# Kernel tuning notes

Hardware: AMD Instinct MI355X
Metric: run time of the kernel (lower is better)

Reference implementation:

```python
import jax, jax.numpy as jnp
import numpy as np

N, P, C = 100000, 48, 8
D, H = 64, 4
DH = D // H
FLAG = 7
EPS = 1e-5


def _layer_norm(x, g, b):
    mu = x.mean(-1, keepdims=True)
    var = ((x - mu) ** 2).mean(-1, keepdims=True)
    return (x - mu) * jax.lax.rsqrt(var + EPS) * g + b


def setup_inputs() -> dict:
    key = jax.random.key(0)
    ks = jax.random.split(key, 24)
    w = lambda k, shp: (jax.random.normal(k, shp, dtype=jnp.float32) * 0.05)
    inp = {
        "voxel_features": jax.random.normal(ks[0], (N, D), dtype=jnp.float32),
        "voxels": jax.random.normal(ks[1], (N, P, C), dtype=jnp.float32),
        "pp_w1": w(ks[2], (D, C)), "pp_b1": w(ks[3], (D,)),
        "pp_w2": w(ks[4], (D, D)), "pp_b2": w(ks[5], (D,)),
        "in_proj_w": w(ks[6], (3 * D, D)), "in_proj_b": w(ks[7], (3 * D,)),
        "out_w": w(ks[8], (D, D)), "out_b": w(ks[9], (D,)),
        "ln1_g": jnp.ones((D,), jnp.float32), "ln1_b": jnp.zeros((D,), jnp.float32),
        "ffn_w1": w(ks[10], (2 * D, D)), "ffn_b1": w(ks[11], (2 * D,)),
        "ffn_w2": w(ks[12], (D, 2 * D)), "ffn_b2": w(ks[13], (D,)),
        "ln2_g": jnp.ones((D,), jnp.float32), "ln2_b": jnp.zeros((D,), jnp.float32),
        "op_w1": w(ks[14], (D, D)), "op_b1": w(ks[15], (D,)),
        "op_w2": w(ks[16], (D, D)), "op_b2": w(ks[17], (D,)),
        "num_points": jax.random.randint(ks[18], (N,), 0, P, dtype=jnp.int32),
    }
    return inp


def reference(voxel_features, voxels, pp_w1, pp_b1, pp_w2, pp_b2,
              in_proj_w, in_proj_b, out_w, out_b, ln1_g, ln1_b,
              ffn_w1, ffn_b1, ffn_w2, ffn_b2, ln2_g, ln2_b,
              op_w1, op_b1, op_w2, op_b2, num_points):
    n, p, _ = voxels.shape
    point_mask = jnp.arange(p)[None, :] < num_points[:, None]          # [N,P]
    current_mask = (voxels[:, :, FLAG] > 0.5) & point_mask             # [N,P]
    history_mask = point_mask & ~current_mask                          # [N,P]
    history_present = history_mask.any(axis=1, keepdims=True)          # [N,1]

    point_features = voxels[:, :, :C]

    def masked_mean(vals, mask):
        m = mask.astype(vals.dtype)[..., None]
        counts = jnp.clip(mask.sum(1, keepdims=True), 1, None).astype(vals.dtype)
        return (vals * m).sum(1) / counts                              # [N,C]

    cur_sum = masked_mean(point_features, current_mask)
    his_sum = masked_mean(point_features, history_mask)

    def point_proj(x):
        return jax.nn.relu(x @ pp_w1.T + pp_b1) @ pp_w2.T + pp_b2

    tokens = jnp.stack([voxel_features, point_proj(cur_sum), point_proj(his_sum)], axis=1)  # [N,3,D]

    key_pad = jnp.stack([jnp.zeros((n,), bool),
                         ~current_mask.any(1),
                         ~history_present[:, 0]], axis=1)              # [N,3]

    # multi-head self-attention over 3 tokens
    qkv = tokens @ in_proj_w.T + in_proj_b                             # [N,3,3D]
    q, k, v = jnp.split(qkv, 3, axis=-1)
    q = q.reshape(n, 3, H, DH).transpose(0, 2, 1, 3)                   # [N,H,3,DH]
    k = k.reshape(n, 3, H, DH).transpose(0, 2, 1, 3)
    v = v.reshape(n, 3, H, DH).transpose(0, 2, 1, 3)
    scores = jnp.einsum('nhqd,nhkd->nhqk', q, k) / np.sqrt(DH)
    scores = jnp.where(key_pad[:, None, None, :], -jnp.inf, scores)
    attn = jax.nn.softmax(scores, axis=-1)
    ctx = jnp.einsum('nhqk,nhkd->nhqd', attn, v)                       # [N,H,3,DH]
    ctx = ctx.transpose(0, 2, 1, 3).reshape(n, 3, D)
    attn_out = ctx @ out_w.T + out_b

    tokens = _layer_norm(tokens + attn_out, ln1_g, ln1_b)
    ffn = jax.nn.relu(tokens @ ffn_w1.T + ffn_b1) @ ffn_w2.T + ffn_b2
    tokens = _layer_norm(tokens + ffn, ln2_g, ln2_b)

    refined = jax.nn.relu(tokens[:, 0] @ op_w1.T + op_b1) @ op_w2.T + op_b2
    refined = refined * history_present.astype(refined.dtype)
    return voxel_features + refined
```

## Files before the change

kernel.cpp:

```cpp
#include <hip/hip_runtime.h>


using bf16x8 = __attribute__((ext_vector_type(8))) __bf16;
using f32x4  = __attribute__((ext_vector_type(4))) float;

#define DEV static __device__ __forceinline__

DEV float bf2f(unsigned short u){
  union { unsigned int i; float f; } v; v.i = ((unsigned int)u) << 16; return v.f;
}
DEV unsigned short f2bf(float f){
  union { float f; unsigned int i; } v; v.f = f;
  unsigned int x = v.i;
  x += 0x7FFFu + ((x >> 16) & 1u);
  return (unsigned short)(x >> 16);
}

DEV unsigned short* lp(unsigned short* base, int row, int col){
  int byte = (col << 1) ^ ((row & 7) << 4);
  return (unsigned short*)((char*)base + (row << 7) + byte);
}

DEV bf16x8 ldA(const unsigned short* base, int mt, int kt, int lane){
  int row = mt*16 + (lane & 15);
  int col = kt*32 + ((lane >> 4) << 3);
  return *(const bf16x8*)lp((unsigned short*)base, row, col);
}
DEV bf16x8 ldB(const unsigned short* w, int frag, int lane){
  return *(const bf16x8*)(w + (size_t)frag*512 + (size_t)lane*8);
}
DEV void stC(unsigned short* base, int mt, int nt, f32x4 c, int lane){
  int col  = nt*16 + (lane & 15);
  int row0 = mt*16 + ((lane >> 4) << 2);
  #pragma unroll
  for (int r = 0; r < 4; ++r) *lp(base, row0 + r, col) = f2bf(c[r]);
}
DEV f32x4 MF(bf16x8 a, bf16x8 b, f32x4 c){
  return __builtin_amdgcn_mfma_f32_16x16x32_bf16(a, b, c, 0, 0, 0);
}

DEV void ld16(const unsigned short* base, int row, int col0, float* o){
  uint4 a = *(const uint4*)lp((unsigned short*)base, row, col0);
  uint4 b = *(const uint4*)lp((unsigned short*)base, row, col0 + 8);
  unsigned int w[8] = {a.x, a.y, a.z, a.w, b.x, b.y, b.z, b.w};
  #pragma unroll
  for (int i = 0; i < 8; ++i){
    union { unsigned int u; float f; } lo, hi;
    lo.u = w[i] << 16; hi.u = w[i] & 0xFFFF0000u;
    o[2*i] = lo.f; o[2*i+1] = hi.f;
  }
}
DEV void st16(unsigned short* base, int row, int col0, const float* f){
  unsigned int w[8];
  #pragma unroll
  for (int i = 0; i < 8; ++i)
    w[i] = (unsigned int)f2bf(f[2*i]) | ((unsigned int)f2bf(f[2*i+1]) << 16);
  *(uint4*)lp(base, row, col0)     = make_uint4(w[0], w[1], w[2], w[3]);
  *(uint4*)lp(base, row, col0 + 8) = make_uint4(w[4], w[5], w[6], w[7]);
}

DEV bf16x8 pack8(const float* f){
  union { bf16x8 v; unsigned short u[8]; } r;
  #pragma unroll
  for (int i = 0; i < 8; ++i) r.u[i] = f2bf(f[i]);
  return r.v;
}

DEV void layer_norm16(f32x4 x[4], const float* g, const float* b, int lane){
  float s[4], s2[4];
  #pragma unroll
  for (int r = 0; r < 4; ++r){
    s[r]  = x[0][r] + x[1][r] + x[2][r] + x[3][r];
    s2[r] = x[0][r]*x[0][r] + x[1][r]*x[1][r] + x[2][r]*x[2][r] + x[3][r]*x[3][r];
  }
  #pragma unroll
  for (int o = 1; o <= 8; o <<= 1){
    #pragma unroll
    for (int r = 0; r < 4; ++r){
      s[r]  += __shfl_xor(s[r],  o);
      s2[r] += __shfl_xor(s2[r], o);
    }
  }
  float mu[4], rs[4];
  #pragma unroll
  for (int r = 0; r < 4; ++r){
    mu[r] = s[r] * (1.f/64.f);
    float var = s2[r] * (1.f/64.f) - mu[r]*mu[r];
    rs[r] = rsqrtf(var + 1e-5f);
  }
  const int cl = lane & 15;
  #pragma unroll
  for (int nt = 0; nt < 4; ++nt){
    float gg = g[nt*16 + cl], bb = b[nt*16 + cl];
    #pragma unroll
    for (int r = 0; r < 4; ++r)
      x[nt][r] = (x[nt][r] - mu[r]) * rs[r] * gg + bb;
  }
}

__global__ void tva_pack_weights(const float* __restrict__ pp_w1, const float* __restrict__ pp_w2,
                                 const float* __restrict__ in_proj_w, const float* __restrict__ out_w,
                                 const float* __restrict__ ffn_w1, const float* __restrict__ ffn_w2,
                                 const float* __restrict__ op_w1, const float* __restrict__ op_w2,
                                 unsigned short* __restrict__ ws)
{
  int b = blockIdx.x, lane = threadIdx.x;
  const float* W; int base, ktiles, K;
  if      (b < 4)  { W = pp_w1;     base = 0;  ktiles = 1; K = 8;   }
  else if (b < 12) { W = pp_w2;     base = 4;  ktiles = 2; K = 64;  }
  else if (b < 36) { W = in_proj_w; base = 12; ktiles = 2; K = 64;  }
  else if (b < 44) { W = out_w;     base = 36; ktiles = 2; K = 64;  }
  else if (b < 60) { W = ffn_w1;    base = 44; ktiles = 2; K = 64;  }
  else if (b < 76) { W = ffn_w2;    base = 60; ktiles = 4; K = 128; }
  else if (b < 84) { W = op_w1;     base = 76; ktiles = 2; K = 64;  }
  else             { W = op_w2;     base = 84; ktiles = 2; K = 64;  }
  int local = b - base;
  int nt = local / ktiles, kt = local % ktiles;
  int n  = nt*16 + (lane & 15);
  int k0 = kt*32 + ((lane >> 4) << 3);
  unsigned short* dst = ws + (size_t)b*512 + (size_t)lane*8;
  #pragma unroll
  for (int i = 0; i < 8; ++i){
    int k = k0 + i;
    float v = (k < K) ? W[(size_t)n*K + k] : 0.0f;
    dst[i] = f2bf(v);
  }
}

__global__ __launch_bounds__(256)
void tva_main(const float* __restrict__ vf, const float* __restrict__ vox,
              const int* __restrict__ num_points,
              const float* __restrict__ pp_b1, const float* __restrict__ pp_b2,
              const float* __restrict__ ipb,  const float* __restrict__ outb,
              const float* __restrict__ ln1g, const float* __restrict__ ln1b,
              const float* __restrict__ f1b,  const float* __restrict__ f2bv,
              const float* __restrict__ ln2g, const float* __restrict__ ln2b,
              const float* __restrict__ o1b,  const float* __restrict__ o2b,
              const unsigned short* __restrict__ wfrag,
              float* __restrict__ out, int nvox)
{
  __shared__ unsigned short smem[4 * 64 * 64];
  const int tid  = threadIdx.x;
  const int wv   = tid >> 6;
  const int lane = tid & 63;
  unsigned short* X = smem + wv * (64*64);
  unsigned short* Q = X + 48*64;

  const int v0 = (blockIdx.x * 4 + wv) * 16;
  if (v0 >= nvox) return;
  const int cl = lane & 15;
  const int r0 = (lane >> 4) << 2;

  const int vi = lane >> 2, pq = lane & 3;
  const int np = num_points[v0 + vi];
  float cs[8] = {0,0,0,0,0,0,0,0}, hs[8] = {0,0,0,0,0,0,0,0};
  float cc = 0.f, hc = 0.f;
  const float4* vp = (const float4*)(vox + (size_t)(v0 + vi) * 384);
  #pragma unroll
  for (int k = 0; k < 12; ++k){
    int p = pq + (k << 2);
    float4 a = vp[p*2], b = vp[p*2 + 1];
    float pm = (p < np) ? 1.f : 0.f;
    float cm = (b.w > 0.5f) ? pm : 0.f;
    float hm = pm - cm;
    cc += cm; hc += hm;
    cs[0] += a.x*cm; cs[1] += a.y*cm; cs[2] += a.z*cm; cs[3] += a.w*cm;
    cs[4] += b.x*cm; cs[5] += b.y*cm; cs[6] += b.z*cm; cs[7] += b.w*cm;
    hs[0] += a.x*hm; hs[1] += a.y*hm; hs[2] += a.z*hm; hs[3] += a.w*hm;
    hs[4] += b.x*hm; hs[5] += b.y*hm; hs[6] += b.z*hm; hs[7] += b.w*hm;
  }
  #pragma unroll
  for (int o = 1; o <= 2; o <<= 1){
    cc += __shfl_xor(cc, o); hc += __shfl_xor(hc, o);
    #pragma unroll
    for (int j = 0; j < 8; ++j){
      cs[j] += __shfl_xor(cs[j], o);
      hs[j] += __shfl_xor(hs[j], o);
    }
  }
  const float icc = 1.f / fmaxf(cc, 1.f);
  const float ihc = 1.f / fmaxf(hc, 1.f);
  const unsigned int myfw = (cc > 0.f ? 1u : 0u) | (hc > 0.f ? 2u : 0u);

  bf16x8 ac, ah;
  {
    const int src = cl * 4;
    float cf[8], hf[8];
    #pragma unroll
    for (int i = 0; i < 8; ++i){
      cf[i] = __shfl(cs[i]*icc, src);
      hf[i] = __shfl(hs[i]*ihc, src);
    }
    union { bf16x8 v; unsigned short u[8]; } rc, rh;
    #pragma unroll
    for (int i = 0; i < 8; ++i){
      rc.u[i] = (lane < 16) ? f2bf(cf[i]) : (unsigned short)0;
      rh.u[i] = (lane < 16) ? f2bf(hf[i]) : (unsigned short)0;
    }
    ac = rc.v; ah = rh.v;
  }

  #pragma unroll
  for (int nt = 0; nt < 4; ++nt){
    float bb = pp_b1[nt*16 + cl];
    f32x4 c0 = {bb, bb, bb, bb}, c1 = {bb, bb, bb, bb};
    bf16x8 B = ldB(wfrag, nt, lane);
    c0 = MF(ac, B, c0);
    c1 = MF(ah, B, c1);
    #pragma unroll
    for (int r = 0; r < 4; ++r){ c0[r] = fmaxf(c0[r], 0.f); c1[r] = fmaxf(c1[r], 0.f); }
    stC(X, 0, nt, c0, lane);
    stC(X, 1, nt, c1, lane);
  }
  {
    bf16x8 hfr[2][2];
    #pragma unroll
    for (int m = 0; m < 2; ++m)
      #pragma unroll
      for (int kt = 0; kt < 2; ++kt) hfr[m][kt] = ldA(X, m, kt, lane);
    #pragma unroll
    for (int m = 0; m < 2; ++m){
      #pragma unroll
      for (int nt = 0; nt < 4; ++nt){
        float bb = pp_b2[nt*16 + cl];
        f32x4 c = {bb, bb, bb, bb};
        c = MF(hfr[m][0], ldB(wfrag, 4 + nt*2 + 0, lane), c);
        c = MF(hfr[m][1], ldB(wfrag, 4 + nt*2 + 1, lane), c);
        stC(X, m, nt, c, lane);
      }
    }
  }

  bf16x8 at[3][2];
  {
    const float* s = vf + (size_t)(v0 + cl) * 64 + ((lane >> 4) << 3);
    #pragma unroll
    for (int kt = 0; kt < 2; ++kt){
      float4 x0 = *(const float4*)(s + kt*32);
      float4 x1 = *(const float4*)(s + kt*32 + 4);
      float f[8] = {x0.x, x0.y, x0.z, x0.w, x1.x, x1.y, x1.z, x1.w};
      at[0][kt] = pack8(f);
    }
    #pragma unroll
    for (int kt = 0; kt < 2; ++kt){
      at[1][kt] = ldA(X, 0, kt, lane);
      at[2][kt] = ldA(X, 1, kt, lane);
    }
  }
  #pragma unroll
  for (int nt = 0; nt < 4; ++nt){
    float bb = ipb[nt*16 + cl];
    f32x4 c = {bb, bb, bb, bb};
    c = MF(at[0][0], ldB(wfrag, 12 + nt*2 + 0, lane), c);
    c = MF(at[0][1], ldB(wfrag, 12 + nt*2 + 1, lane), c);
    #pragma unroll
    for (int r = 0; r < 4; ++r) c[r] *= 0.25f;
    stC(Q, 0, nt, c, lane);
  }
  #pragma unroll
  for (int m = 0; m < 3; ++m){
    #pragma unroll
    for (int nt = 0; nt < 4; ++nt){
      int ntg = 4 + nt;
      float bb = ipb[64 + nt*16 + cl];
      f32x4 c = {bb, bb, bb, bb};
      c = MF(at[m][0], ldB(wfrag, 12 + ntg*2 + 0, lane), c);
      c = MF(at[m][1], ldB(wfrag, 12 + ntg*2 + 1, lane), c);
      stC(X, m, nt, c, lane);
    }
  }

  const int av = cl, hh2 = lane >> 4;
  float p0, p1, p2;
  {
    unsigned int fw = (unsigned int)__shfl((int)myfw, av*4);
    bool caZ = (fw & 1u) != 0, hpZ = (fw & 2u) != 0;
    float q[16]; ld16(Q, av, hh2*16, q);
    float sc[3];
    #pragma unroll
    for (int m = 0; m < 3; ++m){
      float kv[16]; ld16(X, m*16 + av, hh2*16, kv);
      float d = 0.f;
      #pragma unroll
      for (int j = 0; j < 16; ++j) d += q[j]*kv[j];
      sc[m] = d;
    }
    float mx = sc[0];
    mx = caZ ? fmaxf(mx, sc[1]) : mx;
    mx = hpZ ? fmaxf(mx, sc[2]) : mx;
    p0 = __expf(sc[0] - mx);
    p1 = caZ ? __expf(sc[1] - mx) : 0.f;
    p2 = hpZ ? __expf(sc[2] - mx) : 0.f;
    float inv = 1.f / (p0 + p1 + p2);
    p0 *= inv; p1 *= inv; p2 *= inv;
  }

  #pragma unroll
  for (int m = 0; m < 3; ++m){
    #pragma unroll
    for (int nt = 0; nt < 4; ++nt){
      int ntg = 8 + nt;
      float bb = ipb[128 + nt*16 + cl];
      f32x4 c = {bb, bb, bb, bb};
      c = MF(at[m][0], ldB(wfrag, 12 + ntg*2 + 0, lane), c);
      c = MF(at[m][1], ldB(wfrag, 12 + ntg*2 + 1, lane), c);
      stC(X, m, nt, c, lane);
    }
  }

  {
    float ctx[16];
    float vv[16];
    ld16(X, av, hh2*16, vv);
    #pragma unroll
    for (int j = 0; j < 16; ++j) ctx[j] = p0*vv[j];
    ld16(X, 16 + av, hh2*16, vv);
    #pragma unroll
    for (int j = 0; j < 16; ++j) ctx[j] += p1*vv[j];
    ld16(X, 32 + av, hh2*16, vv);
    #pragma unroll
    for (int j = 0; j < 16; ++j) ctx[j] += p2*vv[j];
    st16(Q, av, hh2*16, ctx);
  }

  f32x4 res1[4];
  {
    bf16x8 a0 = ldA(Q, 0, 0, lane), a1 = ldA(Q, 0, 1, lane);
    float rv[16];
    #pragma unroll
    for (int nt = 0; nt < 4; ++nt)
      #pragma unroll
      for (int r = 0; r < 4; ++r)
        rv[nt*4 + r] = vf[(size_t)(v0 + r0 + r)*64 + nt*16 + cl];
    #pragma unroll
    for (int nt = 0; nt < 4; ++nt){
      float bb = outb[nt*16 + cl];
      f32x4 c = {bb, bb, bb, bb};
      c = MF(a0, ldB(wfrag, 36 + nt*2 + 0, lane), c);
      c = MF(a1, ldB(wfrag, 36 + nt*2 + 1, lane), c);
      #pragma unroll
      for (int r = 0; r < 4; ++r) c[r] += rv[nt*4 + r];
      res1[nt] = c;
    }
    layer_norm16(res1, ln1g, ln1b, lane);
    #pragma unroll
    for (int nt = 0; nt < 4; ++nt) stC(Q, 0, nt, res1[nt], lane);
  }

  f32x4 tk2[4];
  {
    bf16x8 a0 = ldA(Q, 0, 0, lane), a1 = ldA(Q, 0, 1, lane);
    #pragma unroll
    for (int nt = 0; nt < 4; ++nt){
      float bb = f2bv[nt*16 + cl];
      tk2[nt] = (f32x4){bb, bb, bb, bb};
    }
    #pragma unroll
    for (int nt = 0; nt < 4; ++nt){
      float bb = f1b[nt*16 + cl];
      f32x4 c = {bb, bb, bb, bb};
      c = MF(a0, ldB(wfrag, 44 + nt*2 + 0, lane), c);
      c = MF(a1, ldB(wfrag, 44 + nt*2 + 1, lane), c);
      #pragma unroll
      for (int r = 0; r < 4; ++r) c[r] = fmaxf(c[r], 0.f);
      stC(X, 0, nt, c, lane);
    }
    {
      bf16x8 h0 = ldA(X, 0, 0, lane), h1 = ldA(X, 0, 1, lane);
      #pragma unroll
      for (int nt = 0; nt < 4; ++nt){
        tk2[nt] = MF(h0, ldB(wfrag, 60 + nt*4 + 0, lane), tk2[nt]);
        tk2[nt] = MF(h1, ldB(wfrag, 60 + nt*4 + 1, lane), tk2[nt]);
      }
    }
    #pragma unroll
    for (int nt = 4; nt < 8; ++nt){
      float bb = f1b[nt*16 + cl];
      f32x4 c = {bb, bb, bb, bb};
      c = MF(a0, ldB(wfrag, 44 + nt*2 + 0, lane), c);
      c = MF(a1, ldB(wfrag, 44 + nt*2 + 1, lane), c);
      #pragma unroll
      for (int r = 0; r < 4; ++r) c[r] = fmaxf(c[r], 0.f);
      stC(X, 0, nt - 4, c, lane);
    }
    {
      bf16x8 h0 = ldA(X, 0, 0, lane), h1 = ldA(X, 0, 1, lane);
      #pragma unroll
      for (int nt = 0; nt < 4; ++nt){
        tk2[nt] = MF(h0, ldB(wfrag, 60 + nt*4 + 2, lane), tk2[nt]);
        tk2[nt] = MF(h1, ldB(wfrag, 60 + nt*4 + 3, lane), tk2[nt]);
      }
    }
    #pragma unroll
    for (int nt = 0; nt < 4; ++nt)
      #pragma unroll
      for (int r = 0; r < 4; ++r) tk2[nt][r] += res1[nt][r];
    layer_norm16(tk2, ln2g, ln2b, lane);
    #pragma unroll
    for (int nt = 0; nt < 4; ++nt) stC(Q, 0, nt, tk2[nt], lane);
  }

  {
    bf16x8 a0 = ldA(Q, 0, 0, lane), a1 = ldA(Q, 0, 1, lane);
    #pragma unroll
    for (int nt = 0; nt < 4; ++nt){
      float bb = o1b[nt*16 + cl];
      f32x4 c = {bb, bb, bb, bb};
      c = MF(a0, ldB(wfrag, 76 + nt*2 + 0, lane), c);
      c = MF(a1, ldB(wfrag, 76 + nt*2 + 1, lane), c);
      #pragma unroll
      for (int r = 0; r < 4; ++r) c[r] = fmaxf(c[r], 0.f);
      stC(X, 0, nt, c, lane);
    }
    bf16x8 b0 = ldA(X, 0, 0, lane), b1 = ldA(X, 0, 1, lane);
    #pragma unroll
    for (int nt = 0; nt < 4; ++nt){
      float bb = o2b[nt*16 + cl];
      f32x4 c = {bb, bb, bb, bb};
      c = MF(b0, ldB(wfrag, 84 + nt*2 + 0, lane), c);
      c = MF(b1, ldB(wfrag, 84 + nt*2 + 1, lane), c);
      #pragma unroll
      for (int r = 0; r < 4; ++r){
        int row = r0 + r;
        unsigned int fw2 = (unsigned int)__shfl((int)myfw, row*4);
        float keep = (fw2 & 2u) ? 1.f : 0.f;
        size_t idx = (size_t)(v0 + row)*64 + nt*16 + cl;
        out[idx] = vf[idx] + keep * c[r];
      }
    }
  }
}

extern "C" void kernel_launch(void* const* d_in, const int* in_sizes, int n_in,
                              void* d_out, int out_size, void* d_ws, size_t ws_size,
                              hipStream_t stream)
{
  (void)n_in; (void)out_size; (void)ws_size;
  const float* vf    = (const float*)d_in[0];
  const float* vox   = (const float*)d_in[1];
  const float* pp_w1 = (const float*)d_in[2];
  const float* pp_b1 = (const float*)d_in[3];
  const float* pp_w2 = (const float*)d_in[4];
  const float* pp_b2 = (const float*)d_in[5];
  const float* ipw   = (const float*)d_in[6];
  const float* ipb   = (const float*)d_in[7];
  const float* outw  = (const float*)d_in[8];
  const float* outb  = (const float*)d_in[9];
  const float* ln1g  = (const float*)d_in[10];
  const float* ln1b  = (const float*)d_in[11];
  const float* f1w   = (const float*)d_in[12];
  const float* f1b   = (const float*)d_in[13];
  const float* f2w   = (const float*)d_in[14];
  const float* f2b   = (const float*)d_in[15];
  const float* ln2g  = (const float*)d_in[16];
  const float* ln2b  = (const float*)d_in[17];
  const float* o1w   = (const float*)d_in[18];
  const float* o1b   = (const float*)d_in[19];
  const float* o2w   = (const float*)d_in[20];
  const float* o2b   = (const float*)d_in[21];
  const int*   npts  = (const int*)d_in[22];
  unsigned short* wfrag = (unsigned short*)d_ws;
  float* out = (float*)d_out;

  const int nvox = in_sizes[0] / 64;
  const int ngrp = nvox / 16;
  const int nblk = (ngrp + 3) / 4;
  tva_pack_weights<<<92, 64, 0, stream>>>(pp_w1, pp_w2, ipw, outw, f1w, f2w, o1w, o2w, wfrag);
  tva_main<<<nblk, 256, 0, stream>>>(vf, vox, npts, pp_b1, pp_b2, ipb, outb,
                                     ln1g, ln1b, f1b, f2b, ln2g, ln2b, o1b, o2b,
                                     wfrag, out, nvox);
}
```

Baseline: 75.09 us.

## Process two 16-voxel groups per wave to reuse weight fragments

Each wave now handles 32 voxels as two 16-voxel groups. Every weight B-fragment loaded for the MFMA stages is reused for both groups, and the voxel reductions for the two groups are interleaved to add instruction-level parallelism. The aim is to halve weight-fragment loads per voxel and hide memory latency better. In exchange, shared memory per block doubles to 64 KB, registers per wave rise, and the grid is half as large, which can reduce occupancy.

```diff
diff --git a/kernel.cpp b/kernel.cpp
--- a/kernel.cpp
+++ b/kernel.cpp
@@ -139,51 +139,54 @@
               const unsigned short* __restrict__ wfrag,
               float* __restrict__ out, int nvox)
 {
-  __shared__ unsigned short smem[4 * 64 * 64];
+  __shared__ unsigned short smem[4 * 2 * 64 * 64];
   const int tid  = threadIdx.x;
   const int wv   = tid >> 6;
   const int lane = tid & 63;
-  unsigned short* X = smem + wv * (64*64);
-  unsigned short* Q = X + 48*64;
-
-  const int v0 = (blockIdx.x * 4 + wv) * 16;
+  unsigned short* Xs[2] = { smem + wv*(2*64*64),             smem + wv*(2*64*64) + 64*64 };
+  unsigned short* Qs[2] = { Xs[0] + 48*64,                   Xs[1] + 48*64 };
+
+  const int v0 = (blockIdx.x * 4 + wv) * 32;
   if (v0 >= nvox) return;
   const int cl = lane & 15;
   const int r0 = (lane >> 4) << 2;
 
   const int vi = lane >> 2, pq = lane & 3;
-  const int np = num_points[v0 + vi];
-  float cs[8] = {0,0,0,0,0,0,0,0}, hs[8] = {0,0,0,0,0,0,0,0};
-  float cc = 0.f, hc = 0.f;
-  const float4* vp = (const float4*)(vox + (size_t)(v0 + vi) * 384);
-  #pragma unroll
-  for (int k = 0; k < 12; ++k){
-    int p = pq + (k << 2);
-    float4 a = vp[p*2], b = vp[p*2 + 1];
-    float pm = (p < np) ? 1.f : 0.f;
-    float cm = (b.w > 0.5f) ? pm : 0.f;
-    float hm = pm - cm;
-    cc += cm; hc += hm;
-    cs[0] += a.x*cm; cs[1] += a.y*cm; cs[2] += a.z*cm; cs[3] += a.w*cm;
-    cs[4] += b.x*cm; cs[5] += b.y*cm; cs[6] += b.z*cm; cs[7] += b.w*cm;
-    hs[0] += a.x*hm; hs[1] += a.y*hm; hs[2] += a.z*hm; hs[3] += a.w*hm;
-    hs[4] += b.x*hm; hs[5] += b.y*hm; hs[6] += b.z*hm; hs[7] += b.w*hm;
-  }
-  #pragma unroll
-  for (int o = 1; o <= 2; o <<= 1){
-    cc += __shfl_xor(cc, o); hc += __shfl_xor(hc, o);
-    #pragma unroll
-    for (int j = 0; j < 8; ++j){
-      cs[j] += __shfl_xor(cs[j], o);
-      hs[j] += __shfl_xor(hs[j], o);
-    }
-  }
-  const float icc = 1.f / fmaxf(cc, 1.f);
-  const float ihc = 1.f / fmaxf(hc, 1.f);
-  const unsigned int myfw = (cc > 0.f ? 1u : 0u) | (hc > 0.f ? 2u : 0u);
-
-  bf16x8 ac, ah;
-  {
+  bf16x8 ac[2], ah[2];
+  unsigned int myfw[2];
+  #pragma unroll
+  for (int g = 0; g < 2; ++g){
+    const int vg = v0 + g*16;
+    const int np = num_points[vg + vi];
+    float cs[8] = {0,0,0,0,0,0,0,0}, hs[8] = {0,0,0,0,0,0,0,0};
+    float cc = 0.f, hc = 0.f;
+    const float4* vp = (const float4*)(vox + (size_t)(vg + vi) * 384);
+    #pragma unroll
+    for (int k = 0; k < 12; ++k){
+      int p = pq + (k << 2);
+      float4 a = vp[p*2], b = vp[p*2 + 1];
+      float pm = (p < np) ? 1.f : 0.f;
+      float cm = (b.w > 0.5f) ? pm : 0.f;
+      float hm = pm - cm;
+      cc += cm; hc += hm;
+      cs[0] += a.x*cm; cs[1] += a.y*cm; cs[2] += a.z*cm; cs[3] += a.w*cm;
+      cs[4] += b.x*cm; cs[5] += b.y*cm; cs[6] += b.z*cm; cs[7] += b.w*cm;
+      hs[0] += a.x*hm; hs[1] += a.y*hm; hs[2] += a.z*hm; hs[3] += a.w*hm;
+      hs[4] += b.x*hm; hs[5] += b.y*hm; hs[6] += b.z*hm; hs[7] += b.w*hm;
+    }
+    #pragma unroll
+    for (int o = 1; o <= 2; o <<= 1){
+      cc += __shfl_xor(cc, o); hc += __shfl_xor(hc, o);
+      #pragma unroll
+      for (int j = 0; j < 8; ++j){
+        cs[j] += __shfl_xor(cs[j], o);
+        hs[j] += __shfl_xor(hs[j], o);
+      }
+    }
+    const float icc = 1.f / fmaxf(cc, 1.f);
+    const float ihc = 1.f / fmaxf(hc, 1.f);
+    myfw[g] = (cc > 0.f ? 1u : 0u) | (hc > 0.f ? 2u : 0u);
+
     const int src = cl * 4;
     float cf[8], hf[8];
     #pragma unroll
@@ -197,89 +200,109 @@
       rc.u[i] = (lane < 16) ? f2bf(cf[i]) : (unsigned short)0;
       rh.u[i] = (lane < 16) ? f2bf(hf[i]) : (unsigned short)0;
     }
-    ac = rc.v; ah = rh.v;
+    ac[g] = rc.v; ah[g] = rh.v;
   }
 
   #pragma unroll
   for (int nt = 0; nt < 4; ++nt){
     float bb = pp_b1[nt*16 + cl];
-    f32x4 c0 = {bb, bb, bb, bb}, c1 = {bb, bb, bb, bb};
     bf16x8 B = ldB(wfrag, nt, lane);
-    c0 = MF(ac, B, c0);
-    c1 = MF(ah, B, c1);
-    #pragma unroll
-    for (int r = 0; r < 4; ++r){ c0[r] = fmaxf(c0[r], 0.f); c1[r] = fmaxf(c1[r], 0.f); }
-    stC(X, 0, nt, c0, lane);
-    stC(X, 1, nt, c1, lane);
+    #pragma unroll
+    for (int g = 0; g < 2; ++g){
+      f32x4 c0 = {bb, bb, bb, bb}, c1 = {bb, bb, bb, bb};
+      c0 = MF(ac[g], B, c0);
+      c1 = MF(ah[g], B, c1);
+      #pragma unroll
+      for (int r = 0; r < 4; ++r){ c0[r] = fmaxf(c0[r], 0.f); c1[r] = fmaxf(c1[r], 0.f); }
+      stC(Xs[g], 0, nt, c0, lane);
+      stC(Xs[g], 1, nt, c1, lane);
+    }
   }
   {
-    bf16x8 hfr[2][2];
-    #pragma unroll
-    for (int m = 0; m < 2; ++m)
-      #pragma unroll
-      for (int kt = 0; kt < 2; ++kt) hfr[m][kt] = ldA(X, m, kt, lane);
-    #pragma unroll
-    for (int m = 0; m < 2; ++m){
-      #pragma unroll
-      for (int nt = 0; nt < 4; ++nt){
-        float bb = pp_b2[nt*16 + cl];
-        f32x4 c = {bb, bb, bb, bb};
-        c = MF(hfr[m][0], ldB(wfrag, 4 + nt*2 + 0, lane), c);
-        c = MF(hfr[m][1], ldB(wfrag, 4 + nt*2 + 1, lane), c);
-        stC(X, m, nt, c, lane);
-      }
-    }
-  }
-
-  bf16x8 at[3][2];
-  {
-    const float* s = vf + (size_t)(v0 + cl) * 64 + ((lane >> 4) << 3);
+    bf16x8 hfr[2][2][2];
+    #pragma unroll
+    for (int g = 0; g < 2; ++g)
+      #pragma unroll
+      for (int m = 0; m < 2; ++m)
+        #pragma unroll
+        for (int kt = 0; kt < 2; ++kt) hfr[g][m][kt] = ldA(Xs[g], m, kt, lane);
+    #pragma unroll
+    for (int nt = 0; nt < 4; ++nt){
+      float bb = pp_b2[nt*16 + cl];
+      bf16x8 B0 = ldB(wfrag, 4 + nt*2 + 0, lane);
+      bf16x8 B1 = ldB(wfrag, 4 + nt*2 + 1, lane);
+      #pragma unroll
+      for (int g = 0; g < 2; ++g)
+        #pragma unroll
+        for (int m = 0; m < 2; ++m){
+          f32x4 c = {bb, bb, bb, bb};
+          c = MF(hfr[g][m][0], B0, c);
+          c = MF(hfr[g][m][1], B1, c);
+          stC(Xs[g], m, nt, c, lane);
+        }
+    }
+  }
+
+  bf16x8 at[2][3][2];
+  #pragma unroll
+  for (int g = 0; g < 2; ++g){
+    const float* s = vf + (size_t)(v0 + g*16 + cl) * 64 + ((lane >> 4) << 3);
     #pragma unroll
     for (int kt = 0; kt < 2; ++kt){
       float4 x0 = *(const float4*)(s + kt*32);
       float4 x1 = *(const float4*)(s + kt*32 + 4);
       float f[8] = {x0.x, x0.y, x0.z, x0.w, x1.x, x1.y, x1.z, x1.w};
-      at[0][kt] = pack8(f);
+      at[g][0][kt] = pack8(f);
     }
     #pragma unroll
     for (int kt = 0; kt < 2; ++kt){
-      at[1][kt] = ldA(X, 0, kt, lane);
-      at[2][kt] = ldA(X, 1, kt, lane);
+      at[g][1][kt] = ldA(Xs[g], 0, kt, lane);
+      at[g][2][kt] = ldA(Xs[g], 1, kt, lane);
     }
   }
   #pragma unroll
   for (int nt = 0; nt < 4; ++nt){
     float bb = ipb[nt*16 + cl];
-    f32x4 c = {bb, bb, bb, bb};
-    c = MF(at[0][0], ldB(wfrag, 12 + nt*2 + 0, lane), c);
-    c = MF(at[0][1], ldB(wfrag, 12 + nt*2 + 1, lane), c);
-    #pragma unroll
-    for (int r = 0; r < 4; ++r) c[r] *= 0.25f;
-    stC(Q, 0, nt, c, lane);
-  }
-  #pragma unroll
-  for (int m = 0; m < 3; ++m){
-    #pragma unroll
-    for (int nt = 0; nt < 4; ++nt){
-      int ntg = 4 + nt;
-      float bb = ipb[64 + nt*16 + cl];
+    bf16x8 B0 = ldB(wfrag, 12 + nt*2 + 0, lane);
+    bf16x8 B1 = ldB(wfrag, 12 + nt*2 + 1, lane);
+    #pragma unroll
+    for (int g = 0; g < 2; ++g){
       f32x4 c = {bb, bb, bb, bb};
-      c = MF(at[m][0], ldB(wfrag, 12 + ntg*2 + 0, lane), c);
-      c = MF(at[m][1], ldB(wfrag, 12 + ntg*2 + 1, lane), c);
-      stC(X, m, nt, c, lane);
-    }
+      c = MF(at[g][0][0], B0, c);
+      c = MF(at[g][0][1], B1, c);
+      #pragma unroll
+      for (int r = 0; r < 4; ++r) c[r] *= 0.25f;
+      stC(Qs[g], 0, nt, c, lane);
+    }
+  }
+  #pragma unroll
+  for (int nt = 0; nt < 4; ++nt){
+    int ntg = 4 + nt;
+    float bb = ipb[64 + nt*16 + cl];
+    bf16x8 B0 = ldB(wfrag, 12 + ntg*2 + 0, lane);
+    bf16x8 B1 = ldB(wfrag, 12 + ntg*2 + 1, lane);
+    #pragma unroll
+    for (int g = 0; g < 2; ++g)
+      #pragma unroll
+      for (int m = 0; m < 3; ++m){
+        f32x4 c = {bb, bb, bb, bb};
+        c = MF(at[g][m][0], B0, c);
+        c = MF(at[g][m][1], B1, c);
+        stC(Xs[g], m, nt, c, lane);
+      }
   }
 
   const int av = cl, hh2 = lane >> 4;
-  float p0, p1, p2;
-  {
-    unsigned int fw = (unsigned int)__shfl((int)myfw, av*4);
+  float p0[2], p1[2], p2[2];
+  #pragma unroll
+  for (int g = 0; g < 2; ++g){
+    unsigned int fw = (unsigned int)__shfl((int)myfw[g], av*4);
     bool caZ = (fw & 1u) != 0, hpZ = (fw & 2u) != 0;
-    float q[16]; ld16(Q, av, hh2*16, q);
+    float q[16]; ld16(Qs[g], av, hh2*16, q);
     float sc[3];
     #pragma unroll
     for (int m = 0; m < 3; ++m){
-      float kv[16]; ld16(X, m*16 + av, hh2*16, kv);
+      float kv[16]; ld16(Xs[g], m*16 + av, hh2*16, kv);
       float d = 0.f;
       #pragma unroll
       for (int j = 0; j < 16; ++j) d += q[j]*kv[j];
@@ -288,144 +311,192 @@
     float mx = sc[0];
     mx = caZ ? fmaxf(mx, sc[1]) : mx;
     mx = hpZ ? fmaxf(mx, sc[2]) : mx;
-    p0 = __expf(sc[0] - mx);
-    p1 = caZ ? __expf(sc[1] - mx) : 0.f;
-    p2 = hpZ ? __expf(sc[2] - mx) : 0.f;
-    float inv = 1.f / (p0 + p1 + p2);
-    p0 *= inv; p1 *= inv; p2 *= inv;
-  }
-
-  #pragma unroll
-  for (int m = 0; m < 3; ++m){
-    #pragma unroll
-    for (int nt = 0; nt < 4; ++nt){
-      int ntg = 8 + nt;
-      float bb = ipb[128 + nt*16 + cl];
-      f32x4 c = {bb, bb, bb, bb};
-      c = MF(at[m][0], ldB(wfrag, 12 + ntg*2 + 0, lane), c);
-      c = MF(at[m][1], ldB(wfrag, 12 + ntg*2 + 1, lane), c);
-      stC(X, m, nt, c, lane);
-    }
-  }
-
-  {
+    float e0 = __expf(sc[0] - mx);
+    float e1 = caZ ? __expf(sc[1] - mx) : 0.f;
+    float e2 = hpZ ? __expf(sc[2] - mx) : 0.f;
+    float inv = 1.f / (e0 + e1 + e2);
+    p0[g] = e0*inv; p1[g] = e1*inv; p2[g] = e2*inv;
+  }
+
+  #pragma unroll
+  for (int nt = 0; nt < 4; ++nt){
+    int ntg = 8 + nt;
+    float bb = ipb[128 + nt*16 + cl];
+    bf16x8 B0 = ldB(wfrag, 12 + ntg*2 + 0, lane);
+    bf16x8 B1 = ldB(wfrag, 12 + ntg*2 + 1, lane);
+    #pragma unroll
+    for (int g = 0; g < 2; ++g)
+      #pragma unroll
+      for (int m = 0; m < 3; ++m){
+        f32x4 c = {bb, bb, bb, bb};
+        c = MF(at[g][m][0], B0, c);
+        c = MF(at[g][m][1], B1, c);
+        stC(Xs[g], m, nt, c, lane);
+      }
+  }
+
+  #pragma unroll
+  for (int g = 0; g < 2; ++g){
     float ctx[16];
     float vv[16];
-    ld16(X, av, hh2*16, vv);
-    #pragma unroll
-    for (int j = 0; j < 16; ++j) ctx[j] = p0*vv[j];
-    ld16(X, 16 + av, hh2*16, vv);
-    #pragma unroll
-    for (int j = 0; j < 16; ++j) ctx[j] += p1*vv[j];
-    ld16(X, 32 + av, hh2*16, vv);
-    #pragma unroll
-    for (int j = 0; j < 16; ++j) ctx[j] += p2*vv[j];
-    st16(Q, av, hh2*16, ctx);
-  }
-
-  f32x4 res1[4];
+    ld16(Xs[g], av, hh2*16, vv);
+    #pragma unroll
+    for (int j = 0; j < 16; ++j) ctx[j] = p0[g]*vv[j];
+    ld16(Xs[g], 16 + av, hh2*16, vv);
+    #pragma unroll
+    for (int j = 0; j < 16; ++j) ctx[j] += p1[g]*vv[j];
+    ld16(Xs[g], 32 + av, hh2*16, vv);
+    #pragma unroll
+    for (int j = 0; j < 16; ++j) ctx[j] += p2[g]*vv[j];
+    st16(Qs[g], av, hh2*16, ctx);
+  }
+
+  f32x4 res1[2][4];
   {
-    bf16x8 a0 = ldA(Q, 0, 0, lane), a1 = ldA(Q, 0, 1, lane);
-    float rv[16];
-    #pragma unroll
-    for (int nt = 0; nt < 4; ++nt)
-      #pragma unroll
-      for (int r = 0; r < 4; ++r)
-        rv[nt*4 + r] = vf[(size_t)(v0 + r0 + r)*64 + nt*16 + cl];
+    bf16x8 a0[2], a1[2];
+    #pragma unroll
+    for (int g = 0; g < 2; ++g){ a0[g] = ldA(Qs[g], 0, 0, lane); a1[g] = ldA(Qs[g], 0, 1, lane); }
     #pragma unroll
     for (int nt = 0; nt < 4; ++nt){
       float bb = outb[nt*16 + cl];
-      f32x4 c = {bb, bb, bb, bb};
-      c = MF(a0, ldB(wfrag, 36 + nt*2 + 0, lane), c);
-      c = MF(a1, ldB(wfrag, 36 + nt*2 + 1, lane), c);
-      #pragma unroll
-      for (int r = 0; r < 4; ++r) c[r] += rv[nt*4 + r];
-      res1[nt] = c;
-    }
-    layer_norm16(res1, ln1g, ln1b, lane);
-    #pragma unroll
-    for (int nt = 0; nt < 4; ++nt) stC(Q, 0, nt, res1[nt], lane);
-  }
-
-  f32x4 tk2[4];
+      bf16x8 B0 = ldB(wfrag, 36 + nt*2 + 0, lane);
+      bf16x8 B1 = ldB(wfrag, 36 + nt*2 + 1, lane);
+      #pragma unroll
+      for (int g = 0; g < 2; ++g){
+        f32x4 c = {bb, bb, bb, bb};
+        c = MF(a0[g], B0, c);
+        c = MF(a1[g], B1, c);
+        #pragma unroll
+        for (int r = 0; r < 4; ++r)
+          c[r] += vf[(size_t)(v0 + g*16 + r0 + r)*64 + nt*16 + cl];
+        res1[g][nt] = c;
+      }
+    }
+    #pragma unroll
+    for (int g = 0; g < 2; ++g){
+      layer_norm16(res1[g], ln1g, ln1b, lane);
+      #pragma unroll
+      for (int nt = 0; nt < 4; ++nt) stC(Qs[g], 0, nt, res1[g][nt], lane);
+    }
+  }
+
+  f32x4 tk2[2][4];
   {
-    bf16x8 a0 = ldA(Q, 0, 0, lane), a1 = ldA(Q, 0, 1, lane);
-    #pragma unroll
-    for (int nt = 0; nt < 4; ++nt){
-      float bb = f2bv[nt*16 + cl];
-      tk2[nt] = (f32x4){bb, bb, bb, bb};
-    }
+    bf16x8 a0[2], a1[2], h0[2], h1[2];
+    #pragma unroll
+    for (int g = 0; g < 2; ++g){ a0[g] = ldA(Qs[g], 0, 0, lane); a1[g] = ldA(Qs[g], 0, 1, lane); }
+    #pragma unroll
+    for (int g = 0; g < 2; ++g)
+      #pragma unroll
+      for (int nt = 0; nt < 4; ++nt){
+        float bb = f2bv[nt*16 + cl];
+        tk2[g][nt] = (f32x4){bb, bb, bb, bb};
+      }
     #pragma unroll
     for (int nt = 0; nt < 4; ++nt){
       float bb = f1b[nt*16 + cl];
-      f32x4 c = {bb, bb, bb, bb};
-      c = MF(a0, ldB(wfrag, 44 + nt*2 + 0, lane), c);
-      c = MF(a1, ldB(wfrag, 44 + nt*2 + 1, lane), c);
-      #pragma unroll
-      for (int r = 0; r < 4; ++r) c[r] = fmaxf(c[r], 0.f);
-      stC(X, 0, nt, c, lane);
-    }
-    {
-      bf16x8 h0 = ldA(X, 0, 0, lane), h1 = ldA(X, 0, 1, lane);
-      #pragma unroll
-      for (int nt = 0; nt < 4; ++nt){
-        tk2[nt] = MF(h0, ldB(wfrag, 60 + nt*4 + 0, lane), tk2[nt]);
-        tk2[nt] = MF(h1, ldB(wfrag, 60 + nt*4 + 1, lane), tk2[nt]);
+      bf16x8 B0 = ldB(wfrag, 44 + nt*2 + 0, lane);
+      bf16x8 B1 = ldB(wfrag, 44 + nt*2 + 1, lane);
+      #pragma unroll
+      for (int g = 0; g < 2; ++g){
+        f32x4 c = {bb, bb, bb, bb};
+        c = MF(a0[g], B0, c);
+        c = MF(a1[g], B1, c);
+        #pragma unroll
+        for (int r = 0; r < 4; ++r) c[r] = fmaxf(c[r], 0.f);
+        stC(Xs[g], 0, nt, c, lane);
+      }
+    }
+    #pragma unroll
+    for (int g = 0; g < 2; ++g){ h0[g] = ldA(Xs[g], 0, 0, lane); h1[g] = ldA(Xs[g], 0, 1, lane); }
+    #pragma unroll
+    for (int nt = 0; nt < 4; ++nt){
+      bf16x8 B0 = ldB(wfrag, 60 + nt*4 + 0, lane);
+      bf16x8 B1 = ldB(wfrag, 60 + nt*4 + 1, lane);
+      #pragma unroll
+      for (int g = 0; g < 2; ++g){
+        tk2[g][nt] = MF(h0[g], B0, tk2[g][nt]);
+        tk2[g][nt] = MF(h1[g], B1, tk2[g][nt]);
       }
     }
     #pragma unroll
     for (int nt = 4; nt < 8; ++nt){
       float bb = f1b[nt*16 + cl];
-      f32x4 c = {bb, bb, bb, bb};
-      c = MF(a0, ldB(wfrag, 44 + nt*2 + 0, lane), c);
-      c = MF(a1, ldB(wfrag, 44 + nt*2 + 1, lane), c);
-      #pragma unroll
-      for (int r = 0; r < 4; ++r) c[r] = fmaxf(c[r], 0.f);
-      stC(X, 0, nt - 4, c, lane);
-    }
-    {
-      bf16x8 h0 = ldA(X, 0, 0, lane), h1 = ldA(X, 0, 1, lane);
-      #pragma unroll
-      for (int nt = 0; nt < 4; ++nt){
-        tk2[nt] = MF(h0, ldB(wfrag, 60 + nt*4 + 2, lane), tk2[nt]);
-        tk2[nt] = MF(h1, ldB(wfrag, 60 + nt*4 + 3, lane), tk2[nt]);
-      }
-    }
-    #pragma unroll
-    for (int nt = 0; nt < 4; ++nt)
-      #pragma unroll
-      for (int r = 0; r < 4; ++r) tk2[nt][r] += res1[nt][r];
-    layer_norm16(tk2, ln2g, ln2b, lane);
-    #pragma unroll
-    for (int nt = 0; nt < 4; ++nt) stC(Q, 0, nt, tk2[nt], lane);
+      bf16x8 B0 = ldB(wfrag, 44 + nt*2 + 0, lane);
+      bf16x8 B1 = ldB(wfrag, 44 + nt*2 + 1, lane);
+      #pragma unroll
+      for (int g = 0; g < 2; ++g){
+        f32x4 c = {bb, bb, bb, bb};
+        c = MF(a0[g], B0, c);
+        c = MF(a1[g], B1, c);
+        #pragma unroll
+        for (int r = 0; r < 4; ++r) c[r] = fmaxf(c[r], 0.f);
+        stC(Xs[g], 0, nt - 4, c, lane);
+      }
+    }
+    #pragma unroll
+    for (int g = 0; g < 2; ++g){ h0[g] = ldA(Xs[g], 0, 0, lane); h1[g] = ldA(Xs[g], 0, 1, lane); }
+    #pragma unroll
+    for (int nt = 0; nt < 4; ++nt){
+      bf16x8 B0 = ldB(wfrag, 60 + nt*4 + 2, lane);
+      bf16x8 B1 = ldB(wfrag, 60 + nt*4 + 3, lane);
+      #pragma unroll
+      for (int g = 0; g < 2; ++g){
+        tk2[g][nt] = MF(h0[g], B0, tk2[g][nt]);
+        tk2[g][nt] = MF(h1[g], B1, tk2[g][nt]);
+      }
+    }
+    #pragma unroll
+    for (int g = 0; g < 2; ++g){
+      #pragma unroll
+      for (int nt = 0; nt < 4; ++nt)
+        #pragma unroll
+        for (int r = 0; r < 4; ++r) tk2[g][nt][r] += res1[g][nt][r];
+      layer_norm16(tk2[g], ln2g, ln2b, lane);
+      #pragma unroll
+      for (int nt = 0; nt < 4; ++nt) stC(Qs[g], 0, nt, tk2[g][nt], lane);
+    }
   }
 
   {
-    bf16x8 a0 = ldA(Q, 0, 0, lane), a1 = ldA(Q, 0, 1, lane);
+    bf16x8 a0[2], a1[2], b0[2], b1[2];
+    #pragma unroll
+    for (int g = 0; g < 2; ++g){ a0[g] = ldA(Qs[g], 0, 0, lane); a1[g] = ldA(Qs[g], 0, 1, lane); }
     #pragma unroll
     for (int nt = 0; nt < 4; ++nt){
       float bb = o1b[nt*16 + cl];
-      f32x4 c = {bb, bb, bb, bb};
-      c = MF(a0, ldB(wfrag, 76 + nt*2 + 0, lane), c);
-      c = MF(a1, ldB(wfrag, 76 + nt*2 + 1, lane), c);
-      #pragma unroll
-      for (int r = 0; r < 4; ++r) c[r] = fmaxf(c[r], 0.f);
-      stC(X, 0, nt, c, lane);
-    }
-    bf16x8 b0 = ldA(X, 0, 0, lane), b1 = ldA(X, 0, 1, lane);
+      bf16x8 B0 = ldB(wfrag, 76 + nt*2 + 0, lane);
+      bf16x8 B1 = ldB(wfrag, 76 + nt*2 + 1, lane);
+      #pragma unroll
+      for (int g = 0; g < 2; ++g){
+        f32x4 c = {bb, bb, bb, bb};
+        c = MF(a0[g], B0, c);
+        c = MF(a1[g], B1, c);
+        #pragma unroll
+        for (int r = 0; r < 4; ++r) c[r] = fmaxf(c[r], 0.f);
+        stC(Xs[g], 0, nt, c, lane);
+      }
+    }
+    #pragma unroll
+    for (int g = 0; g < 2; ++g){ b0[g] = ldA(Xs[g], 0, 0, lane); b1[g] = ldA(Xs[g], 0, 1, lane); }
     #pragma unroll
     for (int nt = 0; nt < 4; ++nt){
       float bb = o2b[nt*16 + cl];
-      f32x4 c = {bb, bb, bb, bb};
-      c = MF(b0, ldB(wfrag, 84 + nt*2 + 0, lane), c);
-      c = MF(b1, ldB(wfrag, 84 + nt*2 + 1, lane), c);
-      #pragma unroll
-      for (int r = 0; r < 4; ++r){
-        int row = r0 + r;
-        unsigned int fw2 = (unsigned int)__shfl((int)myfw, row*4);
-        float keep = (fw2 & 2u) ? 1.f : 0.f;
-        size_t idx = (size_t)(v0 + row)*64 + nt*16 + cl;
-        out[idx] = vf[idx] + keep * c[r];
+      bf16x8 B0 = ldB(wfrag, 84 + nt*2 + 0, lane);
+      bf16x8 B1 = ldB(wfrag, 84 + nt*2 + 1, lane);
+      #pragma unroll
+      for (int g = 0; g < 2; ++g){
+        f32x4 c = {bb, bb, bb, bb};
+        c = MF(b0[g], B0, c);
+        c = MF(b1[g], B1, c);
+        #pragma unroll
+        for (int r = 0; r < 4; ++r){
+          int row = r0 + r;
+          unsigned int fw2 = (unsigned int)__shfl((int)myfw[g], row*4);
+          float keep = (fw2 & 2u) ? 1.f : 0.f;
+          size_t idx = (size_t)(v0 + g*16 + row)*64 + nt*16 + cl;
+          out[idx] = vf[idx] + keep * c[r];
+        }
       }
     }
   }
@@ -462,9 +533,9 @@
   unsigned short* wfrag = (unsigned short*)d_ws;
   float* out = (float*)d_out;
 
-  const int nvox = in_sizes[0] / 64;
-  const int ngrp = nvox / 16;
-  const int nblk = (ngrp + 3) / 4;
+  const int nvox  = in_sizes[0] / 64;
+  const int ndual = nvox / 32;
+  const int nblk  = (ndual + 3) / 4;
   tva_pack_weights<<<92, 64, 0, stream>>>(pp_w1, pp_w2, ipw, outw, f1w, f2w, o1w, o2w, wfrag);
   tva_main<<<nblk, 256, 0, stream>>>(vf, vox, npts, pp_b1, pp_b2, ipb, outb,
                                      ln1g, ln1b, f1b, f2b, ln2g, ln2b, o1b, o2b,
```

Result: slower. 77.89 us (+3.7%).
